# Optimization experiments

Measured on AMD Instinct MI355X. Metric: run time of the kernel, lower is better.

## Reference

```python
import jax, jax.numpy as jnp
import numpy as np

N = 100000
E = 3200000
F_IN, F1, F2, F3, FB, NC = 256, 64, 32, 16, 8, 10


def setup_inputs() -> dict:
    key = jax.random.key(0)
    ks = jax.random.split(key, 12)
    features = jax.random.normal(ks[0], (N, F_IN), dtype=jnp.float32)
    edge_index = jax.random.randint(ks[1], (2, E), 0, N, dtype=jnp.int64)
    def glorot(k, shape):
        lim = np.sqrt(6.0 / (shape[0] + shape[1]))
        return jax.random.uniform(k, shape, jnp.float32, -lim, lim)
    return {
        "features": features,
        "edge_index": edge_index,
        "W1": glorot(ks[2], (F_IN, F1)), "b1": jnp.zeros((F1,), jnp.float32),
        "W2": glorot(ks[3], (F1, F2)),  "b2": jnp.zeros((F2,), jnp.float32),
        "W3": glorot(ks[4], (F2, F3)),  "b3": jnp.zeros((F3,), jnp.float32),
        "Wf": glorot(ks[5], (F3, FB)),  "bf": jnp.zeros((FB,), jnp.float32),
        "Ws": glorot(ks[6], (FB, NC)),  "bs": jnp.zeros((NC,), jnp.float32),
    }


def _gcn_norm(edge_index, n):
    # symmetric normalization with self-loops: deg includes +1 for self-loop
    src, dst = edge_index[0], edge_index[1]
    ones = jnp.ones((edge_index.shape[1],), jnp.float32)
    deg = jax.ops.segment_sum(ones, dst, num_segments=n) + 1.0
    dinv = jax.lax.rsqrt(deg)
    edge_w = dinv[src] * dinv[dst]        # [E]
    self_w = dinv * dinv                   # [N], self-loop weight
    return src, dst, edge_w, self_w


def _gcn_conv(x, W, b, src, dst, edge_w, self_w, n):
    xw = x @ W                                         # [N, Fout]
    msg = xw[src] * edge_w[:, None]                    # gather + scale
    agg = jax.ops.segment_sum(msg, dst, num_segments=n)
    return agg + xw * self_w[:, None] + b


def reference(features, edge_index, W1, b1, W2, b2, W3, b3, Wf, bf, Ws, bs):
    n = features.shape[0]
    src, dst, edge_w, self_w = _gcn_norm(edge_index, n)
    h = jax.nn.relu(_gcn_conv(features, W1, b1, src, dst, edge_w, self_w, n))
    h = jax.nn.relu(_gcn_conv(h, W2, b2, src, dst, edge_w, self_w, n))
    h = jax.nn.relu(_gcn_conv(h, W3, b3, src, dst, edge_w, self_w, n))
    pooled = jnp.mean(h, axis=0, keepdims=True)        # [1, F3]
    hidden = jax.nn.relu(pooled @ Wf + bf)
    scores = hidden @ Ws + bs
    return jax.nn.log_softmax(scores, axis=1)
```

## Files before the change

kernel.cpp:

```cpp
#include <hip/hip_runtime.h>
#include <hip/hip_fp16.h>
#include <math.h>

#define TPB 256
#define BKT_SHIFT 9
#define BKT_N 512
#define NB_MAX 256
#define CHUNK 4096
#define CAP   24576
#define Y_SCALE 16.0f
#define Y_INV_SCALE (1.0f / 16.0f)

typedef short bf16x8 __attribute__((ext_vector_type(8)));
typedef float f32x4  __attribute__((ext_vector_type(4)));

static __device__ inline unsigned short f2bf(float f) {
    union { float f; unsigned u; } v; v.f = f;
    unsigned r = v.u + 0x7FFF + ((v.u >> 16) & 1);
    return (unsigned short)(r >> 16);
}

static __device__ inline unsigned char f2fp8(float x) {
    int p = __builtin_amdgcn_cvt_pk_fp8_f32(x, x, 0, false);
    return (unsigned char)(p & 0xFF);
}

__global__ __launch_bounds__(256) void init_cursor(int* __restrict__ bcursor, int nbkt) {
    int t = threadIdx.x;
    if (t < nbkt) bcursor[t] = t * CAP;
}

__global__ __launch_bounds__(TPB) void bucket_scatter(
    const int* __restrict__ src, const int* __restrict__ dst,
    int* __restrict__ bcursor, unsigned int* __restrict__ packed, int E, int nbkt)
{
    __shared__ unsigned int  spk[CHUNK];
    __shared__ unsigned char sbk[CHUNK];
    __shared__ int h[NB_MAX];
    __shared__ int base[NB_MAX];
    for (int c0 = blockIdx.x * CHUNK; c0 < E; c0 += gridDim.x * CHUNK) {
        int m = min(CHUNK, E - c0);
        for (int i = threadIdx.x; i < nbkt; i += TPB) h[i] = 0;
        __syncthreads();
        for (int i = threadIdx.x; i < m; i += TPB) {
            int d = dst[c0 + i];
            int s = src[c0 + i];
            int b = d >> BKT_SHIFT;
            spk[i] = ((unsigned)(d & (BKT_N - 1)) << 17) | (unsigned)s;
            sbk[i] = (unsigned char)b;
            atomicAdd(&h[b], 1);
        }
        __syncthreads();
        for (int i = threadIdx.x; i < nbkt; i += TPB) {
            int c = h[i];
            base[i] = c ? atomicAdd(&bcursor[i], c) : 0;
            h[i] = 0;
        }
        __syncthreads();
        for (int i = threadIdx.x; i < m; i += TPB) {
            int b = sbk[i];
            int pos = base[b] + atomicAdd(&h[b], 1);
            packed[pos] = spk[i];
        }
        __syncthreads();
    }
}

__global__ __launch_bounds__(256) void bucket_offsets(
    const int* __restrict__ bcursor, int* __restrict__ boff, int nbkt, int E)
{
    int t = threadIdx.x;
    int v = (t < nbkt) ? (bcursor[t] - t * CAP) : 0;
    __shared__ int tmp[256];
    tmp[t] = v; __syncthreads();
    for (int s = 1; s < 256; s <<= 1) {
        int x = (t >= s) ? tmp[t - s] : 0;
        __syncthreads();
        tmp[t] += x;
        __syncthreads();
    }
    if (t < nbkt) boff[t] = tmp[t] - v;
    if (t == 0) boff[nbkt] = E;
}

__global__ __launch_bounds__(256) void bucket_csr(
    const unsigned int* __restrict__ packed, const int* __restrict__ boff,
    int* __restrict__ off, float* __restrict__ dinv, int* __restrict__ ssrc,
    int n, int nbkt)
{
    const int b   = blockIdx.x;
    const int e0  = boff[b];
    const int cnt = boff[b + 1] - e0;
    const int p0  = b * CAP;
    const int v0  = b << BKT_SHIFT;
    const int nv  = min(BKT_N, n - v0);
    const int t   = threadIdx.x;

    __shared__ int hist[BKT_N];
    __shared__ int cur[BKT_N];
    __shared__ int tmp[256];

    for (int i = t; i < nv; i += 256) hist[i] = 0;
    __syncthreads();
    for (int e = t; e < cnt; e += 256)
        atomicAdd(&hist[packed[p0 + e] >> 17], 1);
    __syncthreads();

    int a = (2 * t     < nv) ? hist[2 * t]     : 0;
    int c = (2 * t + 1 < nv) ? hist[2 * t + 1] : 0;
    int ps = a + c;
    tmp[t] = ps; __syncthreads();
    for (int s = 1; s < 256; s <<= 1) {
        int x = (t >= s) ? tmp[t - s] : 0;
        __syncthreads();
        tmp[t] += x;
        __syncthreads();
    }
    int ex = tmp[t] - ps;
    if (2 * t < nv) {
        cur[2 * t] = ex;
        off[v0 + 2 * t] = e0 + ex;
        dinv[v0 + 2 * t] = rsqrtf((float)a + 1.0f);
    }
    if (2 * t + 1 < nv) {
        cur[2 * t + 1] = ex + a;
        off[v0 + 2 * t + 1] = e0 + ex + a;
        dinv[v0 + 2 * t + 1] = rsqrtf((float)c + 1.0f);
    }
    if (b == nbkt - 1 && t == 0) off[n] = boff[nbkt];
    __syncthreads();

    for (int e = t; e < cnt; e += 256) {
        unsigned p = packed[p0 + e];
        int dl = p >> 17;
        int s  = p & 0x1FFFF;
        int pos = atomicAdd(&cur[dl], 1);
        ssrc[e0 + pos] = s;
    }
}

__global__ __launch_bounds__(256) void conv_w(
    const float* __restrict__ W, unsigned short* __restrict__ Wt, int K, int N)
{
    int total = K * N;
    for (int i = threadIdx.x + blockIdx.x * 256; i < total; i += gridDim.x * 256) {
        int k = i / N, c = i % N;
        Wt[c * K + k] = f2bf(W[i]);
    }
}

template<int K, int NCOL, typename AT>
__global__ __launch_bounds__(TPB) void gemm_mfma(
    const AT* __restrict__ A, const unsigned short* __restrict__ Wt,
    const float* __restrict__ dinv, unsigned char* __restrict__ Yq, int n)
{
    constexpr int NT = NCOL / 16;
    constexpr int KS = K / 32;
    const int lane = threadIdx.x & 63;
    const int w    = threadIdx.x >> 6;
    const int rowbase = blockIdx.x * 128 + w * 32;
    const int arow = lane & 15;
    const int kb   = (lane >> 4) * 8;

    f32x4 acc[2][NT];
#pragma unroll
    for (int mt = 0; mt < 2; mt++)
#pragma unroll
        for (int nt = 0; nt < NT; nt++) acc[mt][nt] = (f32x4)(0.f);

#pragma unroll
    for (int ks = 0; ks < KS; ks++) {
        bf16x8 a[2];
#pragma unroll
        for (int mt = 0; mt < 2; mt++) {
            int r = rowbase + mt * 16 + arow;
            if constexpr (sizeof(AT) == 4) {
                if (r < n) {
                    const float4* p = (const float4*)(A + (size_t)r * K + ks * 32 + kb);
                    float4 u = p[0], v = p[1];
                    a[mt][0] = f2bf(u.x); a[mt][1] = f2bf(u.y);
                    a[mt][2] = f2bf(u.z); a[mt][3] = f2bf(u.w);
                    a[mt][4] = f2bf(v.x); a[mt][5] = f2bf(v.y);
                    a[mt][6] = f2bf(v.z); a[mt][7] = f2bf(v.w);
                } else {
#pragma unroll
                    for (int i = 0; i < 8; i++) a[mt][i] = 0;
                }
            } else {
                if (r < n)
                    a[mt] = *(const bf16x8*)(A + (size_t)r * K + ks * 32 + kb);
                else {
#pragma unroll
                    for (int i = 0; i < 8; i++) a[mt][i] = 0;
                }
            }
        }
        bf16x8 b[NT];
#pragma unroll
        for (int nt = 0; nt < NT; nt++)
            b[nt] = *(const bf16x8*)(Wt + (size_t)(nt * 16 + arow) * K + ks * 32 + kb);
#pragma unroll
        for (int mt = 0; mt < 2; mt++)
#pragma unroll
            for (int nt = 0; nt < NT; nt++)
                acc[mt][nt] = __builtin_amdgcn_mfma_f32_16x16x32_bf16(
                    a[mt], b[nt], acc[mt][nt], 0, 0, 0);
    }

#pragma unroll
    for (int mt = 0; mt < 2; mt++) {
        int r0 = rowbase + mt * 16 + (lane >> 4) * 4;
#pragma unroll
        for (int j = 0; j < 4; j++) {
            int r = r0 + j;
            if (r < n) {
                float dv = dinv[r] * Y_SCALE;
#pragma unroll
                for (int nt = 0; nt < NT; nt++)
                    Yq[(size_t)r * NCOL + nt * 16 + arow] = f2fp8(acc[mt][nt][j] * dv);
            }
        }
    }
}

template<int F, bool POOL>
__global__ __launch_bounds__(TPB) void seg_node(
    const int* __restrict__ off, const int* __restrict__ ssrc,
    const unsigned char* __restrict__ Yq, const float* __restrict__ dinv,
    const float* __restrict__ bias, unsigned int* __restrict__ H,
    float* __restrict__ pooled, int n)
{
    constexpr int NU = F / 4;
    constexpr int U  = 4;
    const int v = blockIdx.x * TPB + threadIdx.x;

    float acc[F];
#pragma unroll
    for (int i = 0; i < F; i++) acc[i] = 0.f;
    float r16[16];
    if constexpr (POOL) {
#pragma unroll
        for (int i = 0; i < 16; i++) r16[i] = 0.f;
    }

    if (v < n) {
        {
            const unsigned int* yp = (const unsigned int*)(Yq + (size_t)v * F);
#pragma unroll
            for (int wn = 0; wn < NU; wn++) {
                unsigned u = yp[wn];
                acc[4 * wn + 0] += __builtin_amdgcn_cvt_f32_fp8(u, 0);
                acc[4 * wn + 1] += __builtin_amdgcn_cvt_f32_fp8(u, 1);
                acc[4 * wn + 2] += __builtin_amdgcn_cvt_f32_fp8(u, 2);
                acc[4 * wn + 3] += __builtin_amdgcn_cvt_f32_fp8(u, 3);
            }
        }
        int e0 = off[v], e1 = off[v + 1];
        int e = e0;
        for (; e + U <= e1; e += U) {
            unsigned rw[U][NU];
#pragma unroll
            for (int k = 0; k < U; k++) {
                const unsigned int* yp = (const unsigned int*)(Yq + (size_t)ssrc[e + k] * F);
#pragma unroll
                for (int wn = 0; wn < NU; wn++) rw[k][wn] = yp[wn];
            }
#pragma unroll
            for (int k = 0; k < U; k++)
#pragma unroll
                for (int wn = 0; wn < NU; wn++) {
                    unsigned u = rw[k][wn];
                    acc[4 * wn + 0] += __builtin_amdgcn_cvt_f32_fp8(u, 0);
                    acc[4 * wn + 1] += __builtin_amdgcn_cvt_f32_fp8(u, 1);
                    acc[4 * wn + 2] += __builtin_amdgcn_cvt_f32_fp8(u, 2);
                    acc[4 * wn + 3] += __builtin_amdgcn_cvt_f32_fp8(u, 3);
                }
        }
        for (; e < e1; e++) {
            const unsigned int* yp = (const unsigned int*)(Yq + (size_t)ssrc[e] * F);
#pragma unroll
            for (int wn = 0; wn < NU; wn++) {
                unsigned u = yp[wn];
                acc[4 * wn + 0] += __builtin_amdgcn_cvt_f32_fp8(u, 0);
                acc[4 * wn + 1] += __builtin_amdgcn_cvt_f32_fp8(u, 1);
                acc[4 * wn + 2] += __builtin_amdgcn_cvt_f32_fp8(u, 2);
                acc[4 * wn + 3] += __builtin_amdgcn_cvt_f32_fp8(u, 3);
            }
        }

        float dv = dinv[v] * Y_INV_SCALE;
        if constexpr (!POOL) {
            unsigned int* hp = H + (size_t)v * (F / 2);
#pragma unroll
            for (int i = 0; i < F; i += 2) {
                float rx = fmaxf(fmaf(acc[i],     dv, bias[i]),     0.f);
                float ry = fmaxf(fmaf(acc[i + 1], dv, bias[i + 1]), 0.f);
                hp[i / 2] = ((unsigned)f2bf(ry) << 16) | (unsigned)f2bf(rx);
            }
        } else {
#pragma unroll
            for (int i = 0; i < 16; i++)
                r16[i] = fmaxf(fmaf(acc[i], dv, bias[i]), 0.f);
        }
    }

    if constexpr (POOL) {
        __shared__ float red[TPB][17];
#pragma unroll
        for (int i = 0; i < 16; i++) red[threadIdx.x][i] = r16[i];
        __syncthreads();
        for (int st = 128; st >= 1; st >>= 1) {
            if (threadIdx.x < st) {
#pragma unroll
                for (int i = 0; i < 16; i++)
                    red[threadIdx.x][i] += red[threadIdx.x + st][i];
            }
            __syncthreads();
        }
        if (threadIdx.x < 16) atomicAdd(&pooled[threadIdx.x], red[0][threadIdx.x]);
    }
}

__global__ void head_kernel(const float* __restrict__ pooled,
                            const float* __restrict__ Wf, const float* __restrict__ bf,
                            const float* __restrict__ Ws, const float* __restrict__ bs,
                            float* __restrict__ out, float invn)
{
    if (threadIdx.x == 0 && blockIdx.x == 0) {
        float p[16], h[8], s[10];
        for (int i = 0; i < 16; i++) p[i] = pooled[i] * invn;
        for (int j = 0; j < 8; j++) {
            float a = bf[j];
            for (int i = 0; i < 16; i++) a = fmaf(p[i], Wf[i * 8 + j], a);
            h[j] = fmaxf(a, 0.f);
        }
        float m = -1e30f;
        for (int c = 0; c < 10; c++) {
            float a = bs[c];
            for (int j = 0; j < 8; j++) a = fmaf(h[j], Ws[j * 10 + c], a);
            s[c] = a;
            m = fmaxf(m, a);
        }
        float lse = 0.f;
        for (int c = 0; c < 10; c++) lse += expf(s[c] - m);
        lse = logf(lse) + m;
        for (int c = 0; c < 10; c++) out[c] = s[c] - lse;
    }
}

static inline size_t align_up(size_t x) { return (x + 255) & ~(size_t)255; }

extern "C" void kernel_launch(void* const* d_in, const int* in_sizes, int n_in,
                              void* d_out, int out_size, void* d_ws, size_t ws_size,
                              hipStream_t stream)
{
    const float* X  = (const float*)d_in[0];
    const int*   ei = (const int*)  d_in[1];
    const float* W1 = (const float*)d_in[2];  const float* b1 = (const float*)d_in[3];
    const float* W2 = (const float*)d_in[4];  const float* b2 = (const float*)d_in[5];
    const float* W3 = (const float*)d_in[6];  const float* b3 = (const float*)d_in[7];
    const float* Wf = (const float*)d_in[8];  const float* bf = (const float*)d_in[9];
    const float* Ws = (const float*)d_in[10]; const float* bs = (const float*)d_in[11];

    const int n = in_sizes[0] / 256;
    const int E = in_sizes[1] / 2;
    const int* src = ei;
    const int* dst = ei + E;
    const int nbkt = (n + BKT_N - 1) / BKT_N;

    char* ws = (char*)d_ws;
    size_t off_b = 0;
    int* bcursor = (int*)(ws + off_b);   off_b += align_up(NB_MAX * 4);
    int* boff    = (int*)(ws + off_b);   off_b += align_up((NB_MAX + 1) * 4);
    float* dinv  = (float*)(ws + off_b); off_b += align_up((size_t)n * 4);
    int* off     = (int*)(ws + off_b);   off_b += align_up((size_t)(n + 1) * 4);
    float* pooled= (float*)(ws + off_b); off_b += align_up(16 * 4);
    unsigned short* Wt1 = (unsigned short*)(ws + off_b); off_b += align_up(64 * 256 * 2);
    unsigned short* Wt2 = (unsigned short*)(ws + off_b); off_b += align_up(32 * 64 * 2);
    unsigned short* Wt3 = (unsigned short*)(ws + off_b); off_b += align_up(16 * 32 * 2);
    unsigned int* packed = (unsigned int*)(ws + off_b); off_b += align_up((size_t)nbkt * CAP * 4);
    int* ssrc    = (int*)(ws + off_b);   off_b += align_up((size_t)E * 4);
    unsigned char* Yq = (unsigned char*)(ws + off_b); off_b += align_up((size_t)n * 64);
    unsigned int* H = (unsigned int*)(ws + off_b); off_b += align_up((size_t)n * 64 * 2);

    hipMemsetAsync(pooled, 0, 16 * 4, stream);

    init_cursor<<<1, 256, 0, stream>>>(bcursor, nbkt);
    int nchunk = (E + CHUNK - 1) / CHUNK;
    bucket_scatter<<<nchunk, TPB, 0, stream>>>(src, dst, bcursor, packed, E, nbkt);
    bucket_offsets<<<1, 256, 0, stream>>>(bcursor, boff, nbkt, E);
    bucket_csr<<<nbkt, 256, 0, stream>>>(packed, boff, off, dinv, ssrc, n, nbkt);

    conv_w<<<16, 256, 0, stream>>>(W1, Wt1, 256, 64);
    conv_w<<<2, 256, 0, stream>>>(W2, Wt2, 64, 32);
    conv_w<<<1, 256, 0, stream>>>(W3, Wt3, 32, 16);

    const int gblk = (n + 127) / 128;
    const int nblk = (n + TPB - 1) / TPB;

    gemm_mfma<256, 64, float><<<gblk, TPB, 0, stream>>>(X, Wt1, dinv, Yq, n);
    seg_node<64, false><<<nblk, TPB, 0, stream>>>(off, ssrc, Yq, dinv, b1, H, nullptr, n);

    gemm_mfma<64, 32, unsigned short><<<gblk, TPB, 0, stream>>>(
        (const unsigned short*)H, Wt2, dinv, Yq, n);
    seg_node<32, false><<<nblk, TPB, 0, stream>>>(off, ssrc, Yq, dinv, b2, H, nullptr, n);

    gemm_mfma<32, 16, unsigned short><<<gblk, TPB, 0, stream>>>(
        (const unsigned short*)H, Wt3, dinv, Yq, n);
    seg_node<16, true><<<nblk, TPB, 0, stream>>>(off, ssrc, Yq, dinv, b3, nullptr, pooled, n);

    head_kernel<<<1, 64, 0, stream>>>(pooled, Wf, bf, Ws, bs, (float*)d_out, 1.0f / (float)n);
}
```

Measured before the change: 274.9 us.

## Split fp8 feature table into column-slabs and aggregate per slab in separate blocks

The GEMM epilogue now writes the fp8 Yq table as column-partitioned slabs (16 or 8 bytes per node per slab) instead of row-major full rows. Aggregation launches one block group per slab, so each gathered row is a single aligned vector load and each thread needs fewer accumulator registers. The goal is a smaller random-gather working set per pass and better occupancy, at the cost of re-reading the CSR offsets and indices once per slab. The pooled reduction also replaces the shared-memory tree with shared atomics.

Result: slower. 355.7 us (+29.4%).

```diff
diff --git a/kernel.cpp b/kernel.cpp
--- a/kernel.cpp
+++ b/kernel.cpp
@@ -23,6 +23,13 @@
 static __device__ inline unsigned char f2fp8(float x) {
     int p = __builtin_amdgcn_cvt_pk_fp8_f32(x, x, 0, false);
     return (unsigned char)(p & 0xFF);
+}
+
+static __device__ inline void acc_word(float* a, unsigned u) {
+    a[0] += __builtin_amdgcn_cvt_f32_fp8(u, 0);
+    a[1] += __builtin_amdgcn_cvt_f32_fp8(u, 1);
+    a[2] += __builtin_amdgcn_cvt_f32_fp8(u, 2);
+    a[3] += __builtin_amdgcn_cvt_f32_fp8(u, 3);
 }
 
 __global__ __launch_bounds__(256) void init_cursor(int* __restrict__ bcursor, int nbkt) {
@@ -215,109 +222,114 @@
             int r = r0 + j;
             if (r < n) {
                 float dv = dinv[r] * Y_SCALE;
-#pragma unroll
-                for (int nt = 0; nt < NT; nt++)
-                    Yq[(size_t)r * NCOL + nt * 16 + arow] = f2fp8(acc[mt][nt][j] * dv);
+                if constexpr (NCOL == 16) {
+                    Yq[((size_t)(arow >> 3) * n + r) * 8 + (arow & 7)] =
+                        f2fp8(acc[mt][0][j] * dv);
+                } else {
+#pragma unroll
+                    for (int nt = 0; nt < NT; nt++)
+                        Yq[((size_t)nt * n + r) * 16 + arow] = f2fp8(acc[mt][nt][j] * dv);
+                }
             }
         }
     }
 }
 
-template<int F, bool POOL>
-__global__ __launch_bounds__(TPB) void seg_node(
+template<int FB, int PARTS, bool POOL>
+__global__ __launch_bounds__(TPB) void seg_part(
     const int* __restrict__ off, const int* __restrict__ ssrc,
     const unsigned char* __restrict__ Yq, const float* __restrict__ dinv,
     const float* __restrict__ bias, unsigned int* __restrict__ H,
     float* __restrict__ pooled, int n)
 {
-    constexpr int NU = F / 4;
-    constexpr int U  = 4;
-    const int v = blockIdx.x * TPB + threadIdx.x;
-
-    float acc[F];
-#pragma unroll
-    for (int i = 0; i < F; i++) acc[i] = 0.f;
-    float r16[16];
+    constexpr int F     = FB * PARTS;
+    constexpr int NU    = FB / 4;
+    constexpr int LOG2P = (PARTS == 4) ? 2 : 1;
+    constexpr int U     = (FB == 8) ? 8 : 4;
+
+    const int part = blockIdx.x & (PARTS - 1);
+    const int v    = (blockIdx.x >> LOG2P) * TPB + threadIdx.x;
+    const unsigned char* yb = Yq + (size_t)part * n * FB;
+
+    __shared__ float pl[16];
     if constexpr (POOL) {
-#pragma unroll
-        for (int i = 0; i < 16; i++) r16[i] = 0.f;
+        if (threadIdx.x < 16) pl[threadIdx.x] = 0.f;
+        __syncthreads();
     }
 
     if (v < n) {
-        {
-            const unsigned int* yp = (const unsigned int*)(Yq + (size_t)v * F);
-#pragma unroll
-            for (int wn = 0; wn < NU; wn++) {
-                unsigned u = yp[wn];
-                acc[4 * wn + 0] += __builtin_amdgcn_cvt_f32_fp8(u, 0);
-                acc[4 * wn + 1] += __builtin_amdgcn_cvt_f32_fp8(u, 1);
-                acc[4 * wn + 2] += __builtin_amdgcn_cvt_f32_fp8(u, 2);
-                acc[4 * wn + 3] += __builtin_amdgcn_cvt_f32_fp8(u, 3);
-            }
-        }
+        float acc[FB];
+#pragma unroll
+        for (int i = 0; i < FB; i++) acc[i] = 0.f;
+
+        if constexpr (NU == 4) {
+            uint4 q = *(const uint4*)(yb + (size_t)v * FB);
+            acc_word(acc + 0, q.x); acc_word(acc + 4, q.y);
+            acc_word(acc + 8, q.z); acc_word(acc + 12, q.w);
+        } else {
+            uint2 q = *(const uint2*)(yb + (size_t)v * FB);
+            acc_word(acc + 0, q.x); acc_word(acc + 4, q.y);
+        }
+
         int e0 = off[v], e1 = off[v + 1];
         int e = e0;
         for (; e + U <= e1; e += U) {
-            unsigned rw[U][NU];
-#pragma unroll
-            for (int k = 0; k < U; k++) {
-                const unsigned int* yp = (const unsigned int*)(Yq + (size_t)ssrc[e + k] * F);
-#pragma unroll
-                for (int wn = 0; wn < NU; wn++) rw[k][wn] = yp[wn];
+            if constexpr (NU == 4) {
+                uint4 rw[U];
+#pragma unroll
+                for (int k = 0; k < U; k++)
+                    rw[k] = *(const uint4*)(yb + (size_t)ssrc[e + k] * FB);
+#pragma unroll
+                for (int k = 0; k < U; k++) {
+                    acc_word(acc + 0, rw[k].x); acc_word(acc + 4, rw[k].y);
+                    acc_word(acc + 8, rw[k].z); acc_word(acc + 12, rw[k].w);
+                }
+            } else {
+                uint2 rw[U];
+#pragma unroll
+                for (int k = 0; k < U; k++)
+                    rw[k] = *(const uint2*)(yb + (size_t)ssrc[e + k] * FB);
+#pragma unroll
+                for (int k = 0; k < U; k++) {
+                    acc_word(acc + 0, rw[k].x); acc_word(acc + 4, rw[k].y);
+                }
             }
-#pragma unroll
-            for (int k = 0; k < U; k++)
-#pragma unroll
-                for (int wn = 0; wn < NU; wn++) {
-                    unsigned u = rw[k][wn];
-                    acc[4 * wn + 0] += __builtin_amdgcn_cvt_f32_fp8(u, 0);
-                    acc[4 * wn + 1] += __builtin_amdgcn_cvt_f32_fp8(u, 1);
-                    acc[4 * wn + 2] += __builtin_amdgcn_cvt_f32_fp8(u, 2);
-                    acc[4 * wn + 3] += __builtin_amdgcn_cvt_f32_fp8(u, 3);
-                }
         }
         for (; e < e1; e++) {
-            const unsigned int* yp = (const unsigned int*)(Yq + (size_t)ssrc[e] * F);
-#pragma unroll
-            for (int wn = 0; wn < NU; wn++) {
-                unsigned u = yp[wn];
-                acc[4 * wn + 0] += __builtin_amdgcn_cvt_f32_fp8(u, 0);
-                acc[4 * wn + 1] += __builtin_amdgcn_cvt_f32_fp8(u, 1);
-                acc[4 * wn + 2] += __builtin_amdgcn_cvt_f32_fp8(u, 2);
-                acc[4 * wn + 3] += __builtin_amdgcn_cvt_f32_fp8(u, 3);
+            if constexpr (NU == 4) {
+                uint4 q = *(const uint4*)(yb + (size_t)ssrc[e] * FB);
+                acc_word(acc + 0, q.x); acc_word(acc + 4, q.y);
+                acc_word(acc + 8, q.z); acc_word(acc + 12, q.w);
+            } else {
+                uint2 q = *(const uint2*)(yb + (size_t)ssrc[e] * FB);
+                acc_word(acc + 0, q.x); acc_word(acc + 4, q.y);
             }
         }
 
         float dv = dinv[v] * Y_INV_SCALE;
         if constexpr (!POOL) {
-            unsigned int* hp = H + (size_t)v * (F / 2);
-#pragma unroll
-            for (int i = 0; i < F; i += 2) {
-                float rx = fmaxf(fmaf(acc[i],     dv, bias[i]),     0.f);
-                float ry = fmaxf(fmaf(acc[i + 1], dv, bias[i + 1]), 0.f);
-                hp[i / 2] = ((unsigned)f2bf(ry) << 16) | (unsigned)f2bf(rx);
+            unsigned hw[FB / 2];
+#pragma unroll
+            for (int i = 0; i < FB; i += 2) {
+                float rx = fmaxf(fmaf(acc[i],     dv, bias[part * FB + i]),     0.f);
+                float ry = fmaxf(fmaf(acc[i + 1], dv, bias[part * FB + i + 1]), 0.f);
+                hw[i / 2] = ((unsigned)f2bf(ry) << 16) | (unsigned)f2bf(rx);
             }
+            unsigned int* hp = H + (size_t)v * (F / 2) + part * (FB / 2);
+#pragma unroll
+            for (int i = 0; i < FB / 2; i += 4)
+                *(uint4*)(hp + i) = make_uint4(hw[i], hw[i + 1], hw[i + 2], hw[i + 3]);
         } else {
 #pragma unroll
-            for (int i = 0; i < 16; i++)
-                r16[i] = fmaxf(fmaf(acc[i], dv, bias[i]), 0.f);
+            for (int i = 0; i < FB; i++)
+                atomicAdd(&pl[part * FB + i],
+                          fmaxf(fmaf(acc[i], dv, bias[part * FB + i]), 0.f));
         }
     }
 
     if constexpr (POOL) {
-        __shared__ float red[TPB][17];
-#pragma unroll
-        for (int i = 0; i < 16; i++) red[threadIdx.x][i] = r16[i];
-        __syncthreads();
-        for (int st = 128; st >= 1; st >>= 1) {
-            if (threadIdx.x < st) {
-#pragma unroll
-                for (int i = 0; i < 16; i++)
-                    red[threadIdx.x][i] += red[threadIdx.x + st][i];
-            }
-            __syncthreads();
-        }
-        if (threadIdx.x < 16) atomicAdd(&pooled[threadIdx.x], red[0][threadIdx.x]);
+        __syncthreads();
+        if (threadIdx.x < 16) atomicAdd(&pooled[threadIdx.x], pl[threadIdx.x]);
     }
 }
 
@@ -399,15 +411,15 @@
     const int nblk = (n + TPB - 1) / TPB;
 
     gemm_mfma<256, 64, float><<<gblk, TPB, 0, stream>>>(X, Wt1, dinv, Yq, n);
-    seg_node<64, false><<<nblk, TPB, 0, stream>>>(off, ssrc, Yq, dinv, b1, H, nullptr, n);
+    seg_part<16, 4, false><<<4 * nblk, TPB, 0, stream>>>(off, ssrc, Yq, dinv, b1, H, nullptr, n);
 
     gemm_mfma<64, 32, unsigned short><<<gblk, TPB, 0, stream>>>(
         (const unsigned short*)H, Wt2, dinv, Yq, n);
-    seg_node<32, false><<<nblk, TPB, 0, stream>>>(off, ssrc, Yq, dinv, b2, H, nullptr, n);
+    seg_part<16, 2, false><<<2 * nblk, TPB, 0, stream>>>(off, ssrc, Yq, dinv, b2, H, nullptr, n);
 
     gemm_mfma<32, 16, unsigned short><<<gblk, TPB, 0, stream>>>(
         (const unsigned short*)H, Wt3, dinv, Yq, n);
-    seg_node<16, true><<<nblk, TPB, 0, stream>>>(off, ssrc, Yq, dinv, b3, nullptr, pooled, n);
+    seg_part<8, 2, true><<<2 * nblk, TPB, 0, stream>>>(off, ssrc, Yq, dinv, b3, nullptr, pooled, n);
 
     head_kernel<<<1, 64, 0, stream>>>(pooled, Wf, bf, Ws, bs, (float*)d_out, 1.0f / (float)n);
 }
```

## Split each node's aggregation across a lane group with shuffled neighbor indices

Applied to the files above, without the earlier changes.

The CSR aggregation for layers one and two now assigns G = F/16 lanes to each destination node. Each lane loads and accumulates a 16-byte slice of every neighbor row, and neighbor indices are loaded cooperatively and shared with __shfl. The old design used one thread per node. The new one launches more parallel work, issues wide uint4 loads, and needs fewer registers per thread. It does cost extra shuffles, and lane groups within a wavefront diverge when degrees differ. The pooling layer keeps one thread per node but switches to uint4 loads.

New measurement: 265.0 us. -3.6%, faster.

```diff
diff --git a/kernel.cpp b/kernel.cpp
--- a/kernel.cpp
+++ b/kernel.cpp
@@ -23,6 +23,13 @@
 static __device__ inline unsigned char f2fp8(float x) {
     int p = __builtin_amdgcn_cvt_pk_fp8_f32(x, x, 0, false);
     return (unsigned char)(p & 0xFF);
+}
+
+static __device__ inline void acc_word(float* a, unsigned u) {
+    a[0] += __builtin_amdgcn_cvt_f32_fp8(u, 0);
+    a[1] += __builtin_amdgcn_cvt_f32_fp8(u, 1);
+    a[2] += __builtin_amdgcn_cvt_f32_fp8(u, 2);
+    a[3] += __builtin_amdgcn_cvt_f32_fp8(u, 3);
 }
 
 __global__ __launch_bounds__(256) void init_cursor(int* __restrict__ bcursor, int nbkt) {
@@ -223,102 +230,131 @@
     }
 }
 
-template<int F, bool POOL>
-__global__ __launch_bounds__(TPB) void seg_node(
+template<int F>
+__global__ __launch_bounds__(TPB) void seg_group(
     const int* __restrict__ off, const int* __restrict__ ssrc,
     const unsigned char* __restrict__ Yq, const float* __restrict__ dinv,
-    const float* __restrict__ bias, unsigned int* __restrict__ H,
-    float* __restrict__ pooled, int n)
-{
-    constexpr int NU = F / 4;
-    constexpr int U  = 4;
+    const float* __restrict__ bias, unsigned int* __restrict__ H, int n)
+{
+    constexpr int G     = F / 16;
+    constexpr int LOG2G = (G == 4) ? 2 : 1;
+    const int lane  = threadIdx.x & 63;
+    const int fl    = lane & (G - 1);
+    const int gbase = lane & ~(G - 1);
+    const int v     = (blockIdx.x * TPB + threadIdx.x) >> LOG2G;
+
+    if (v >= n) return;
+
+    float acc[16];
+#pragma unroll
+    for (int i = 0; i < 16; i++) acc[i] = 0.f;
+
+    {
+        uint4 q = *(const uint4*)(Yq + (size_t)v * F + fl * 16);
+        acc_word(acc + 0, q.x); acc_word(acc + 4, q.y);
+        acc_word(acc + 8, q.z); acc_word(acc + 12, q.w);
+    }
+
+    const int e0 = off[v], e1 = off[v + 1];
+    int e = e0;
+    for (; e + G <= e1; e += G) {
+        int idx = ssrc[e + fl];
+        uint4 q[G];
+#pragma unroll
+        for (int k = 0; k < G; k++) {
+            int sj = __shfl(idx, gbase + k, 64);
+            q[k] = *(const uint4*)(Yq + (size_t)sj * F + fl * 16);
+        }
+#pragma unroll
+        for (int k = 0; k < G; k++) {
+            acc_word(acc + 0, q[k].x); acc_word(acc + 4, q[k].y);
+            acc_word(acc + 8, q[k].z); acc_word(acc + 12, q[k].w);
+        }
+    }
+    int rem = e1 - e;
+    if (rem > 0) {
+        int idx = (fl < rem) ? ssrc[e + fl] : 0;
+        for (int k = 0; k < rem; k++) {
+            int sj = __shfl(idx, gbase + k, 64);
+            uint4 q = *(const uint4*)(Yq + (size_t)sj * F + fl * 16);
+            acc_word(acc + 0, q.x); acc_word(acc + 4, q.y);
+            acc_word(acc + 8, q.z); acc_word(acc + 12, q.w);
+        }
+    }
+
+    float dv = dinv[v] * Y_INV_SCALE;
+    unsigned hw[8];
+#pragma unroll
+    for (int i = 0; i < 16; i += 2) {
+        float rx = fmaxf(fmaf(acc[i],     dv, bias[fl * 16 + i]),     0.f);
+        float ry = fmaxf(fmaf(acc[i + 1], dv, bias[fl * 16 + i + 1]), 0.f);
+        hw[i / 2] = ((unsigned)f2bf(ry) << 16) | (unsigned)f2bf(rx);
+    }
+    unsigned int* hp = H + (size_t)v * (F / 2) + fl * 8;
+    *(uint4*)(hp + 0) = make_uint4(hw[0], hw[1], hw[2], hw[3]);
+    *(uint4*)(hp + 4) = make_uint4(hw[4], hw[5], hw[6], hw[7]);
+}
+
+__global__ __launch_bounds__(TPB) void seg_pool16(
+    const int* __restrict__ off, const int* __restrict__ ssrc,
+    const unsigned char* __restrict__ Yq, const float* __restrict__ dinv,
+    const float* __restrict__ bias, float* __restrict__ pooled, int n)
+{
+    constexpr int U = 4;
     const int v = blockIdx.x * TPB + threadIdx.x;
 
-    float acc[F];
-#pragma unroll
-    for (int i = 0; i < F; i++) acc[i] = 0.f;
     float r16[16];
-    if constexpr (POOL) {
-#pragma unroll
-        for (int i = 0; i < 16; i++) r16[i] = 0.f;
-    }
+#pragma unroll
+    for (int i = 0; i < 16; i++) r16[i] = 0.f;
 
     if (v < n) {
+        float acc[16];
+#pragma unroll
+        for (int i = 0; i < 16; i++) acc[i] = 0.f;
+
         {
-            const unsigned int* yp = (const unsigned int*)(Yq + (size_t)v * F);
-#pragma unroll
-            for (int wn = 0; wn < NU; wn++) {
-                unsigned u = yp[wn];
-                acc[4 * wn + 0] += __builtin_amdgcn_cvt_f32_fp8(u, 0);
-                acc[4 * wn + 1] += __builtin_amdgcn_cvt_f32_fp8(u, 1);
-                acc[4 * wn + 2] += __builtin_amdgcn_cvt_f32_fp8(u, 2);
-                acc[4 * wn + 3] += __builtin_amdgcn_cvt_f32_fp8(u, 3);
-            }
+            uint4 q = *(const uint4*)(Yq + (size_t)v * 16);
+            acc_word(acc + 0, q.x); acc_word(acc + 4, q.y);
+            acc_word(acc + 8, q.z); acc_word(acc + 12, q.w);
         }
         int e0 = off[v], e1 = off[v + 1];
         int e = e0;
         for (; e + U <= e1; e += U) {
-            unsigned rw[U][NU];
+            uint4 q[U];
+#pragma unroll
+            for (int k = 0; k < U; k++)
+                q[k] = *(const uint4*)(Yq + (size_t)ssrc[e + k] * 16);
 #pragma unroll
             for (int k = 0; k < U; k++) {
-                const unsigned int* yp = (const unsigned int*)(Yq + (size_t)ssrc[e + k] * F);
-#pragma unroll
-                for (int wn = 0; wn < NU; wn++) rw[k][wn] = yp[wn];
+                acc_word(acc + 0, q[k].x); acc_word(acc + 4, q[k].y);
+                acc_word(acc + 8, q[k].z); acc_word(acc + 12, q[k].w);
             }
-#pragma unroll
-            for (int k = 0; k < U; k++)
-#pragma unroll
-                for (int wn = 0; wn < NU; wn++) {
-                    unsigned u = rw[k][wn];
-                    acc[4 * wn + 0] += __builtin_amdgcn_cvt_f32_fp8(u, 0);
-                    acc[4 * wn + 1] += __builtin_amdgcn_cvt_f32_fp8(u, 1);
-                    acc[4 * wn + 2] += __builtin_amdgcn_cvt_f32_fp8(u, 2);
-                    acc[4 * wn + 3] += __builtin_amdgcn_cvt_f32_fp8(u, 3);
-                }
         }
         for (; e < e1; e++) {
-            const unsigned int* yp = (const unsigned int*)(Yq + (size_t)ssrc[e] * F);
-#pragma unroll
-            for (int wn = 0; wn < NU; wn++) {
-                unsigned u = yp[wn];
-                acc[4 * wn + 0] += __builtin_amdgcn_cvt_f32_fp8(u, 0);
-                acc[4 * wn + 1] += __builtin_amdgcn_cvt_f32_fp8(u, 1);
-                acc[4 * wn + 2] += __builtin_amdgcn_cvt_f32_fp8(u, 2);
-                acc[4 * wn + 3] += __builtin_amdgcn_cvt_f32_fp8(u, 3);
-            }
+            uint4 q = *(const uint4*)(Yq + (size_t)ssrc[e] * 16);
+            acc_word(acc + 0, q.x); acc_word(acc + 4, q.y);
+            acc_word(acc + 8, q.z); acc_word(acc + 12, q.w);
         }
 
         float dv = dinv[v] * Y_INV_SCALE;
-        if constexpr (!POOL) {
-            unsigned int* hp = H + (size_t)v * (F / 2);
-#pragma unroll
-            for (int i = 0; i < F; i += 2) {
-                float rx = fmaxf(fmaf(acc[i],     dv, bias[i]),     0.f);
-                float ry = fmaxf(fmaf(acc[i + 1], dv, bias[i + 1]), 0.f);
-                hp[i / 2] = ((unsigned)f2bf(ry) << 16) | (unsigned)f2bf(rx);
-            }
-        } else {
+#pragma unroll
+        for (int i = 0; i < 16; i++)
+            r16[i] = fmaxf(fmaf(acc[i], dv, bias[i]), 0.f);
+    }
+
+    __shared__ float red[TPB][17];
+#pragma unroll
+    for (int i = 0; i < 16; i++) red[threadIdx.x][i] = r16[i];
+    __syncthreads();
+    for (int st = 128; st >= 1; st >>= 1) {
+        if (threadIdx.x < st) {
 #pragma unroll
             for (int i = 0; i < 16; i++)
-                r16[i] = fmaxf(fmaf(acc[i], dv, bias[i]), 0.f);
-        }
-    }
-
-    if constexpr (POOL) {
-        __shared__ float red[TPB][17];
-#pragma unroll
-        for (int i = 0; i < 16; i++) red[threadIdx.x][i] = r16[i];
-        __syncthreads();
-        for (int st = 128; st >= 1; st >>= 1) {
-            if (threadIdx.x < st) {
-#pragma unroll
-                for (int i = 0; i < 16; i++)
-                    red[threadIdx.x][i] += red[threadIdx.x + st][i];
-            }
-            __syncthreads();
-        }
-        if (threadIdx.x < 16) atomicAdd(&pooled[threadIdx.x], red[0][threadIdx.x]);
-    }
+                red[threadIdx.x][i] += red[threadIdx.x + st][i];
+        }
+        __syncthreads();
+    }
+    if (threadIdx.x < 16) atomicAdd(&pooled[threadIdx.x], red[0][threadIdx.x]);
 }
 
 __global__ void head_kernel(const float* __restrict__ pooled,
@@ -399,15 +435,15 @@
     const int nblk = (n + TPB - 1) / TPB;
 
     gemm_mfma<256, 64, float><<<gblk, TPB, 0, stream>>>(X, Wt1, dinv, Yq, n);
-    seg_node<64, false><<<nblk, TPB, 0, stream>>>(off, ssrc, Yq, dinv, b1, H, nullptr, n);
+    seg_group<64><<<(4 * n + TPB - 1) / TPB, TPB, 0, stream>>>(off, ssrc, Yq, dinv, b1, H, n);
 
     gemm_mfma<64, 32, unsigned short><<<gblk, TPB, 0, stream>>>(
         (const unsigned short*)H, Wt2, dinv, Yq, n);
-    seg_node<32, false><<<nblk, TPB, 0, stream>>>(off, ssrc, Yq, dinv, b2, H, nullptr, n);
+    seg_group<32><<<(2 * n + TPB - 1) / TPB, TPB, 0, stream>>>(off, ssrc, Yq, dinv, b2, H, n);
 
     gemm_mfma<32, 16, unsigned short><<<gblk, TPB, 0, stream>>>(
         (const unsigned short*)H, Wt3, dinv, Yq, n);
-    seg_node<16, true><<<nblk, TPB, 0, stream>>>(off, ssrc, Yq, dinv, b3, nullptr, pooled, n);
+    seg_pool16<<<nblk, TPB, 0, stream>>>(off, ssrc, Yq, dinv, b3, pooled, n);
 
     head_kernel<<<1, 64, 0, stream>>>(pooled, Wf, bf, Ws, bs, (float*)d_out, 1.0f / (float)n);
 }
```
